# Kernel optimization log

Hardware: AMD Instinct MI355X
Metric: run time of the kernel (lower is better)

## Reference

```python
import jax, jax.numpy as jnp
import numpy as np

D_MODEL = 4096
D_BASE = 8192
K_SUB = 1024
N_TOK = 8192


def setup_inputs() -> dict:
    key = jax.random.key(0)
    k1, k2, k3, k4 = jax.random.split(key, 4)
    x = jax.random.normal(k1, (N_TOK, D_MODEL), dtype=jnp.float32)
    subspace_indices = jax.random.randint(k2, (K_SUB,), 0, D_BASE)
    # learned shared basis (orthogonal init approximated by scaled gaussian)
    U_base = jax.random.normal(k3, (D_MODEL, D_BASE), dtype=jnp.float32) / np.sqrt(D_MODEL)
    V_base = jax.random.normal(k4, (D_BASE, D_MODEL), dtype=jnp.float32) / np.sqrt(D_BASE)
    return {"x": x, "subspace_indices": subspace_indices, "U_base": U_base, "V_base": V_base}


def reference(x, subspace_indices, U_base, V_base):
    # gather active subspace columns/rows of the shared basis
    u_subset = U_base[:, subspace_indices]          # [d_model, k]
    v_subset = V_base[subspace_indices, :]          # [k, d_model]
    projected = jax.nn.silu(x @ u_subset)           # [n_tok, k]
    return projected @ v_subset                     # [n_tok, d_model]
```

## Files before the change

kernel.cpp:

```cpp
#include <hip/hip_runtime.h>
#include <hip/hip_bf16.h>
#include <stdint.h>

#define D_MODEL 4096
#define D_BASE  8192
#define K_SUB   1024
#define N_TOK   8192

typedef __attribute__((ext_vector_type(8))) short bf16x8;
typedef __attribute__((ext_vector_type(4))) float f32x4;

__device__ __forceinline__ unsigned short f2bf(float f) {
    union { float f; uint32_t u; } c; c.f = f;
    uint32_t u = c.u;
    uint32_t r = u + 0x7FFFu + ((u >> 16) & 1u);
    return (unsigned short)(r >> 16);
}

__device__ __forceinline__ void gload_lds16(const void* g, void* l) {
    __builtin_amdgcn_global_load_lds(
        (__attribute__((address_space(1))) void*)g,
        (__attribute__((address_space(3))) void*)l, 16, 0, 0);
}

#define VMCNT(N) do { __builtin_amdgcn_sched_barrier(0); \
    asm volatile("s_waitcnt vmcnt(" #N ")" ::: "memory"); } while (0)
#define PHASE_MID() do { __builtin_amdgcn_sched_barrier(0); __builtin_amdgcn_s_barrier(); \
    asm volatile("s_waitcnt lgkmcnt(0)" ::: "memory"); __builtin_amdgcn_sched_barrier(0); } while (0)
#define PHASE_END() do { __builtin_amdgcn_sched_barrier(0); __builtin_amdgcn_s_barrier(); } while (0)

__global__ __launch_bounds__(256) void prep_fused(const float* __restrict__ x,
                                                  const int* __restrict__ idx,
                                                  const float* __restrict__ U,
                                                  const float* __restrict__ V,
                                                  unsigned short* __restrict__ xb,
                                                  unsigned short* __restrict__ Ut,
                                                  unsigned short* __restrict__ Vt) {
    __shared__ __align__(16) char smem[8704];
    const int b = blockIdx.x;
    const int t = threadIdx.x;
    if (b < 2048) {
        unsigned short* tile = (unsigned short*)smem;
        const int n0 = (b & 3) * 256;
        const int k0 = (b >> 2) * 8;
        const int n = n0 + t;
        const int col = idx[n];
        const float* Ucol = U + (size_t)k0 * D_BASE + col;
        #pragma unroll
        for (int kr = 0; kr < 8; ++kr)
            tile[t * 12 + kr] = f2bf(Ucol[(size_t)kr * D_BASE]);
        __syncthreads();
        ushort4 a = *(const ushort4*)&tile[t * 12];
        ushort4 q = *(const ushort4*)&tile[t * 12 + 4];
        *(ushort4*)(Ut + (size_t)n * D_MODEL + k0) = a;
        *(ushort4*)(Ut + (size_t)n * D_MODEL + k0 + 4) = q;
    } else if (b < 3072) {
        unsigned short (*tile)[66] = (unsigned short(*)[66])smem;
        int* lidx = (int*)(smem + 64 * 66 * 2);
        const int bx = b - 2048;
        const int n0 = (bx & 15) * 64;
        const int d0 = (bx >> 4) * 64;
        if (t < 64) lidx[t] = idx[n0 + t];
        __syncthreads();
        const int c = t & 63, r4 = t >> 6;
        #pragma unroll
        for (int p = 0; p < 16; ++p) {
            int nr = p * 4 + r4;
            tile[nr][c] = f2bf(V[(size_t)lidx[nr] * D_MODEL + d0 + c]);
        }
        __syncthreads();
        #pragma unroll
        for (int p = 0; p < 16; ++p) {
            int dr = p * 4 + r4;
            Vt[(size_t)(d0 + dr) * K_SUB + n0 + c] = tile[c][dr];
        }
    } else {
        const int cb = b - 3072;
        int e = cb * 256 + t;
        const float4* p = (const float4*)x + (size_t)e * 2;
        float4 a = p[0], q = p[1];
        ushort4 lo, hi;
        lo.x = f2bf(a.x); lo.y = f2bf(a.y); lo.z = f2bf(a.z); lo.w = f2bf(a.w);
        hi.x = f2bf(q.x); hi.y = f2bf(q.y); hi.z = f2bf(q.z); hi.w = f2bf(q.w);
        *(ushort4*)(xb + (size_t)e * 8) = lo;
        *(ushort4*)(xb + (size_t)e * 8 + 4) = hi;
    }
}

__global__ __launch_bounds__(512, 2)
void gemm1_8p(const unsigned short* __restrict__ A, const unsigned short* __restrict__ Bt,
              unsigned short* __restrict__ C) {
    constexpr int K = D_MODEL, N = K_SUB, NT = K / 64;
    __shared__ __align__(16) unsigned short lds[49152];

    const int t = threadIdx.x, lane = t & 63, w = t >> 6;
    const int wm = w >> 1, wn = w & 1;
    const int lr = lane & 15, lk = lane >> 4;

    const int f = blockIdx.x;
    const int g = (f & 7) * 32 + (f >> 3);
    const int m0 = (g >> 3) * 256, n0 = (g & 7) * 128;

    const int cswz0 = ((lk ^ (lr & 7)) * 8);
    const int cswz1 = (((4 + lk) ^ (lr & 7)) * 8);
    const int srow = lane >> 3;
    const int scol = ((lane & 7) ^ srow) * 8;

    auto stage_A = [&](int kt, int half) {
        const unsigned short* src = A + (size_t)(m0 + half * 128) * K + kt * 64;
        unsigned short* dst = &lds[(kt & 1) * 24576 + half * 8192];
        #pragma unroll
        for (int i = 0; i < 2; ++i) {
            int c2 = i * 8 + w;
            gload_lds16(src + (size_t)(c2 * 8 + srow) * K + scol, dst + c2 * 512);
        }
    };
    auto stage_B = [&](int kt) {
        const unsigned short* src = Bt + (size_t)n0 * K + kt * 64;
        unsigned short* dst = &lds[(kt & 1) * 24576 + 16384];
        #pragma unroll
        for (int i = 0; i < 2; ++i) {
            int c2 = i * 8 + w;
            gload_lds16(src + (size_t)(c2 * 8 + srow) * K + scol, dst + c2 * 512);
        }
    };
    auto read_A = [&](int kt, bf16x8 (&af)[4][2]) {
        const unsigned short* base = &lds[(kt & 1) * 24576 + (wm >> 1) * 8192];
        #pragma unroll
        for (int m = 0; m < 4; ++m) {
            int rw = (wm & 1) * 64 + m * 16 + lr;
            af[m][0] = *(const bf16x8*)(base + rw * 64 + cswz0);
            af[m][1] = *(const bf16x8*)(base + rw * 64 + cswz1);
        }
    };
    auto read_B2 = [&](int kt, int nh, bf16x8 (&bfr)[2][2]) {
        const unsigned short* base = &lds[(kt & 1) * 24576 + 16384];
        #pragma unroll
        for (int n = 0; n < 2; ++n) {
            int rw = wn * 64 + (nh * 2 + n) * 16 + lr;
            bfr[n][0] = *(const bf16x8*)(base + rw * 64 + cswz0);
            bfr[n][1] = *(const bf16x8*)(base + rw * 64 + cswz1);
        }
    };

    f32x4 acc[4][4] = {};

    stage_A(0, 0); stage_A(0, 1); stage_B(0); stage_A(1, 0);
    VMCNT(2);
    __builtin_amdgcn_s_barrier();
    __builtin_amdgcn_sched_barrier(0);

    for (int kt = 0; kt < NT; kt += 2) {
        const bool more = (kt + 2 < NT);
        {
            bf16x8 af[4][2], bfr[2][2];
            read_A(kt, af); read_B2(kt, 0, bfr);
            stage_A(kt + 1, 1); stage_B(kt + 1);
            PHASE_MID();
            __builtin_amdgcn_s_setprio(1);
            #pragma unroll
            for (int m = 0; m < 4; ++m)
                #pragma unroll
                for (int n = 0; n < 2; ++n)
                    #pragma unroll
                    for (int ks = 0; ks < 2; ++ks)
                        acc[m][n] = __builtin_amdgcn_mfma_f32_16x16x32_bf16(
                            af[m][ks], bfr[n][ks], acc[m][n], 0, 0, 0);
            __builtin_amdgcn_s_setprio(0);
            PHASE_END();
            bf16x8 bfr2[2][2];
            read_B2(kt, 1, bfr2);
            if (more) stage_A(kt + 2, 0);
            PHASE_MID();
            __builtin_amdgcn_s_setprio(1);
            #pragma unroll
            for (int m = 0; m < 4; ++m)
                #pragma unroll
                for (int n = 0; n < 2; ++n)
                    #pragma unroll
                    for (int ks = 0; ks < 2; ++ks)
                        acc[m][2 + n] = __builtin_amdgcn_mfma_f32_16x16x32_bf16(
                            af[m][ks], bfr2[n][ks], acc[m][2 + n], 0, 0, 0);
            __builtin_amdgcn_s_setprio(0);
            if (more) { VMCNT(2); } else { VMCNT(0); }
            PHASE_END();
        }
        {
            bf16x8 af[4][2], bfr[2][2];
            read_A(kt + 1, af); read_B2(kt + 1, 0, bfr);
            if (more) { stage_A(kt + 2, 1); stage_B(kt + 2); }
            PHASE_MID();
            __builtin_amdgcn_s_setprio(1);
            #pragma unroll
            for (int m = 0; m < 4; ++m)
                #pragma unroll
                for (int n = 0; n < 2; ++n)
                    #pragma unroll
                    for (int ks = 0; ks < 2; ++ks)
                        acc[m][n] = __builtin_amdgcn_mfma_f32_16x16x32_bf16(
                            af[m][ks], bfr[n][ks], acc[m][n], 0, 0, 0);
            __builtin_amdgcn_s_setprio(0);
            PHASE_END();
            bf16x8 bfr2[2][2];
            read_B2(kt + 1, 1, bfr2);
            if (more) stage_A(kt + 3, 0);
            PHASE_MID();
            __builtin_amdgcn_s_setprio(1);
            #pragma unroll
            for (int m = 0; m < 4; ++m)
                #pragma unroll
                for (int n = 0; n < 2; ++n)
                    #pragma unroll
                    for (int ks = 0; ks < 2; ++ks)
                        acc[m][2 + n] = __builtin_amdgcn_mfma_f32_16x16x32_bf16(
                            af[m][ks], bfr2[n][ks], acc[m][2 + n], 0, 0, 0);
            __builtin_amdgcn_s_setprio(0);
            if (more) VMCNT(2);
            PHASE_END();
        }
    }

    #pragma unroll
    for (int m = 0; m < 4; ++m)
        #pragma unroll
        for (int n = 0; n < 4; ++n)
            #pragma unroll
            for (int r = 0; r < 4; ++r) {
                int row = m0 + wm * 64 + m * 16 + lk * 4 + r;
                int col = n0 + wn * 64 + n * 16 + lr;
                float v = acc[m][n][r];
                v = v / (1.0f + __expf(-v));
                C[(size_t)row * N + col] = f2bf(v);
            }
}

__global__ __launch_bounds__(512, 2)
void gemm2_8p(const unsigned short* __restrict__ A, const unsigned short* __restrict__ Bt,
              float* __restrict__ C) {
    constexpr int K = K_SUB, N = D_MODEL, NT = K / 64;
    constexpr int BUFSZ = 32768;
    __shared__ __align__(16) unsigned short lds[2 * BUFSZ];

    const int t = threadIdx.x, lane = t & 63, w = t >> 6;
    const int wr = w >> 2, wc = w & 3;
    const int lr = lane & 15, lk = lane >> 4;

    const int f = blockIdx.x;
    const int g = (f & 7) * 64 + (f >> 3);
    const int m0 = (g >> 4) * 256, n0 = (g & 15) * 256;

    const int cswz0 = ((lk ^ (lr & 7)) * 8);
    const int cswz1 = (((4 + lk) ^ (lr & 7)) * 8);
    const int srow = lane >> 3;
    const int scol = ((lane & 7) ^ srow) * 8;

    auto stage_A = [&](int kt, int mh) {
        const unsigned short* src = A + (size_t)(m0 + mh * 128) * K + kt * 64;
        unsigned short* dst = &lds[(kt & 1) * BUFSZ + mh * 8192];
        #pragma unroll
        for (int i = 0; i < 2; ++i) {
            int c2 = i * 8 + w;
            gload_lds16(src + (size_t)(c2 * 8 + srow) * K + scol, dst + c2 * 512);
        }
    };
    auto stage_B = [&](int kt, int nh) {
        const unsigned short* src = Bt + (size_t)(n0 + nh * 128) * K + kt * 64;
        unsigned short* dst = &lds[(kt & 1) * BUFSZ + 16384 + nh * 8192];
        #pragma unroll
        for (int i = 0; i < 2; ++i) {
            int c2 = i * 8 + w;
            gload_lds16(src + (size_t)(c2 * 8 + srow) * K + scol, dst + c2 * 512);
        }
    };
    auto read_A = [&](int kt, int mh, bf16x8 (&af)[4][2]) {
        const unsigned short* base = &lds[(kt & 1) * BUFSZ + mh * 8192];
        #pragma unroll
        for (int m = 0; m < 4; ++m) {
            int rw = wr * 64 + m * 16 + lr;
            af[m][0] = *(const bf16x8*)(base + rw * 64 + cswz0);
            af[m][1] = *(const bf16x8*)(base + rw * 64 + cswz1);
        }
    };
    auto read_B = [&](int kt, int nh, bf16x8 (&bfr)[2][2]) {
        const unsigned short* base = &lds[(kt & 1) * BUFSZ + 16384 + nh * 8192];
        #pragma unroll
        for (int n = 0; n < 2; ++n) {
            int rw = wc * 32 + n * 16 + lr;
            bfr[n][0] = *(const bf16x8*)(base + rw * 64 + cswz0);
            bfr[n][1] = *(const bf16x8*)(base + rw * 64 + cswz1);
        }
    };

    f32x4 acc[8][4] = {};

    stage_A(0, 0); stage_B(0, 0); stage_B(0, 1); stage_A(0, 1);
    stage_A(1, 0); stage_B(1, 1); stage_A(1, 1);
    VMCNT(6);
    __builtin_amdgcn_s_barrier();
    __builtin_amdgcn_sched_barrier(0);

    for (int kt = 0; kt < NT; ++kt) {
        bf16x8 af[4][2], bf0[2][2], bf1[2][2];
        {
            read_A(kt, 0, af); read_B(kt, 0, bf0);
            if (kt + 1 < NT) stage_B(kt + 1, 0);
            PHASE_MID();
            __builtin_amdgcn_s_setprio(1);
            #pragma unroll
            for (int m = 0; m < 4; ++m)
                #pragma unroll
                for (int n = 0; n < 2; ++n)
                    #pragma unroll
                    for (int ks = 0; ks < 2; ++ks)
                        acc[m][n] = __builtin_amdgcn_mfma_f32_16x16x32_bf16(
                            af[m][ks], bf0[n][ks], acc[m][n], 0, 0, 0);
            __builtin_amdgcn_s_setprio(0);
            PHASE_END();
        }
        {
            read_B(kt, 1, bf1);
            if (kt + 2 < NT) stage_A(kt + 2, 0);
            PHASE_MID();
            __builtin_amdgcn_s_setprio(1);
            #pragma unroll
            for (int m = 0; m < 4; ++m)
                #pragma unroll
                for (int n = 0; n < 2; ++n)
                    #pragma unroll
                    for (int ks = 0; ks < 2; ++ks)
                        acc[m][2 + n] = __builtin_amdgcn_mfma_f32_16x16x32_bf16(
                            af[m][ks], bf1[n][ks], acc[m][2 + n], 0, 0, 0);
            __builtin_amdgcn_s_setprio(0);
            PHASE_END();
        }
        {
            read_A(kt, 1, af);
            if (kt + 2 < NT) stage_B(kt + 2, 1);
            PHASE_MID();
            __builtin_amdgcn_s_setprio(1);
            #pragma unroll
            for (int m = 0; m < 4; ++m)
                #pragma unroll
                for (int n = 0; n < 2; ++n)
                    #pragma unroll
                    for (int ks = 0; ks < 2; ++ks)
                        acc[4 + m][n] = __builtin_amdgcn_mfma_f32_16x16x32_bf16(
                            af[m][ks], bf0[n][ks], acc[4 + m][n], 0, 0, 0);
            __builtin_amdgcn_s_setprio(0);
            PHASE_END();
        }
        {
            if (kt + 2 < NT) stage_A(kt + 2, 1);
            PHASE_MID();
            __builtin_amdgcn_s_setprio(1);
            #pragma unroll
            for (int m = 0; m < 4; ++m)
                #pragma unroll
                for (int n = 0; n < 2; ++n)
                    #pragma unroll
                    for (int ks = 0; ks < 2; ++ks)
                        acc[4 + m][2 + n] = __builtin_amdgcn_mfma_f32_16x16x32_bf16(
                            af[m][ks], bf1[n][ks], acc[4 + m][2 + n], 0, 0, 0);
            __builtin_amdgcn_s_setprio(0);
            __builtin_amdgcn_sched_barrier(0);
            if (kt < NT - 2) { VMCNT(6); }
            else if (kt == NT - 2) { VMCNT(0); }
            PHASE_END();
        }
    }

    #pragma unroll
    for (int mh = 0; mh < 2; ++mh)
        #pragma unroll
        for (int nh = 0; nh < 2; ++nh)
            #pragma unroll
            for (int m = 0; m < 4; ++m)
                #pragma unroll
                for (int n = 0; n < 2; ++n)
                    #pragma unroll
                    for (int r = 0; r < 4; ++r) {
                        int row = m0 + mh * 128 + wr * 64 + m * 16 + lk * 4 + r;
                        int col = n0 + nh * 128 + wc * 32 + n * 16 + lr;
                        C[(size_t)row * N + col] = acc[mh * 4 + m][nh * 2 + n][r];
                    }
}

extern "C" void kernel_launch(void* const* d_in, const int* in_sizes, int n_in,
                              void* d_out, int out_size, void* d_ws, size_t ws_size,
                              hipStream_t stream) {
    const float* x   = (const float*)d_in[0];
    const int*   idx = (const int*)d_in[1];
    const float* U   = (const float*)d_in[2];
    const float* V   = (const float*)d_in[3];
    float* out = (float*)d_out;

    unsigned short* Ut = (unsigned short*)d_ws;
    unsigned short* Vt = Ut + (size_t)K_SUB * D_MODEL;
    unsigned short* P  = Vt + (size_t)K_SUB * D_MODEL;
    unsigned short* xb = (unsigned short*)d_out;

    prep_fused<<<2048 + 1024 + 16384, 256, 0, stream>>>(x, idx, U, V, xb, Ut, Vt);
    gemm1_8p<<<256, 512, 0, stream>>>(xb, Ut, P);
    gemm2_8p<<<512, 512, 0, stream>>>(P, Vt, out);
}
```

Baseline: 231.3 us.

## Fuse fp32-to-bf16 conversion of x into first GEMM's A-tile load

Removes the separate conversion pass over x in the prep kernel. The first GEMM now loads fp32 x tiles into registers, converts them to bf16 and writes them swizzled into LDS, with a one-stage register prefetch. This saves writing and re-reading a 64 MB bf16 copy of x. In exchange the GEMM reads twice the bytes for A per tile, cannot use direct global-to-LDS loads for A, and carries more registers, with the occupancy hint in the launch bounds dropped. It also removes the LDS round trip in the U gather.

```diff
diff --git a/kernel.cpp b/kernel.cpp
--- a/kernel.cpp
+++ b/kernel.cpp
@@ -8,6 +8,7 @@
 #define N_TOK   8192
 
 typedef __attribute__((ext_vector_type(8))) short bf16x8;
+typedef __attribute__((ext_vector_type(8))) unsigned short u16x8;
 typedef __attribute__((ext_vector_type(4))) float f32x4;
 
 __device__ __forceinline__ unsigned short f2bf(float f) {
@@ -29,32 +30,30 @@
     asm volatile("s_waitcnt lgkmcnt(0)" ::: "memory"); __builtin_amdgcn_sched_barrier(0); } while (0)
 #define PHASE_END() do { __builtin_amdgcn_sched_barrier(0); __builtin_amdgcn_s_barrier(); } while (0)
 
-__global__ __launch_bounds__(256) void prep_fused(const float* __restrict__ x,
-                                                  const int* __restrict__ idx,
+__global__ __launch_bounds__(256) void prep_fused(const int* __restrict__ idx,
                                                   const float* __restrict__ U,
                                                   const float* __restrict__ V,
-                                                  unsigned short* __restrict__ xb,
                                                   unsigned short* __restrict__ Ut,
                                                   unsigned short* __restrict__ Vt) {
     __shared__ __align__(16) char smem[8704];
     const int b = blockIdx.x;
     const int t = threadIdx.x;
     if (b < 2048) {
-        unsigned short* tile = (unsigned short*)smem;
         const int n0 = (b & 3) * 256;
         const int k0 = (b >> 2) * 8;
         const int n = n0 + t;
         const int col = idx[n];
         const float* Ucol = U + (size_t)k0 * D_BASE + col;
+        unsigned short v[8];
         #pragma unroll
         for (int kr = 0; kr < 8; ++kr)
-            tile[t * 12 + kr] = f2bf(Ucol[(size_t)kr * D_BASE]);
-        __syncthreads();
-        ushort4 a = *(const ushort4*)&tile[t * 12];
-        ushort4 q = *(const ushort4*)&tile[t * 12 + 4];
+            v[kr] = f2bf(Ucol[(size_t)kr * D_BASE]);
+        ushort4 a, q;
+        a.x = v[0]; a.y = v[1]; a.z = v[2]; a.w = v[3];
+        q.x = v[4]; q.y = v[5]; q.z = v[6]; q.w = v[7];
         *(ushort4*)(Ut + (size_t)n * D_MODEL + k0) = a;
         *(ushort4*)(Ut + (size_t)n * D_MODEL + k0 + 4) = q;
-    } else if (b < 3072) {
+    } else {
         unsigned short (*tile)[66] = (unsigned short(*)[66])smem;
         int* lidx = (int*)(smem + 64 * 66 * 2);
         const int bx = b - 2048;
@@ -74,28 +73,19 @@
             int dr = p * 4 + r4;
             Vt[(size_t)(d0 + dr) * K_SUB + n0 + c] = tile[c][dr];
         }
-    } else {
-        const int cb = b - 3072;
-        int e = cb * 256 + t;
-        const float4* p = (const float4*)x + (size_t)e * 2;
-        float4 a = p[0], q = p[1];
-        ushort4 lo, hi;
-        lo.x = f2bf(a.x); lo.y = f2bf(a.y); lo.z = f2bf(a.z); lo.w = f2bf(a.w);
-        hi.x = f2bf(q.x); hi.y = f2bf(q.y); hi.z = f2bf(q.z); hi.w = f2bf(q.w);
-        *(ushort4*)(xb + (size_t)e * 8) = lo;
-        *(ushort4*)(xb + (size_t)e * 8 + 4) = hi;
     }
 }
 
-__global__ __launch_bounds__(512, 2)
-void gemm1_8p(const unsigned short* __restrict__ A, const unsigned short* __restrict__ Bt,
-              unsigned short* __restrict__ C) {
+__global__ __launch_bounds__(512)
+void gemm1_f(const float* __restrict__ A, const unsigned short* __restrict__ Bt,
+             unsigned short* __restrict__ C) {
     constexpr int K = D_MODEL, N = K_SUB, NT = K / 64;
     __shared__ __align__(16) unsigned short lds[49152];
 
     const int t = threadIdx.x, lane = t & 63, w = t >> 6;
     const int wm = w >> 1, wn = w & 1;
     const int lr = lane & 15, lk = lane >> 4;
+    const int rt = t >> 1, ch = t & 1;
 
     const int f = blockIdx.x;
     const int g = (f & 7) * 32 + (f >> 3);
@@ -106,13 +96,23 @@
     const int srow = lane >> 3;
     const int scol = ((lane & 7) ^ srow) * 8;
 
-    auto stage_A = [&](int kt, int half) {
-        const unsigned short* src = A + (size_t)(m0 + half * 128) * K + kt * 64;
-        unsigned short* dst = &lds[(kt & 1) * 24576 + half * 8192];
-        #pragma unroll
-        for (int i = 0; i < 2; ++i) {
-            int c2 = i * 8 + w;
-            gload_lds16(src + (size_t)(c2 * 8 + srow) * K + scol, dst + c2 * 512);
+    auto issue_A = [&](int kt, f32x4 (&ar)[8]) {
+        const float* src = A + (size_t)(m0 + rt) * K + kt * 64 + ch * 32;
+        #pragma unroll
+        for (int j = 0; j < 8; ++j)
+            ar[j] = *(const f32x4*)(src + j * 4);
+    };
+    auto write_A = [&](int kt, const f32x4 (&ar)[8]) {
+        unsigned short* dst = &lds[(kt & 1) * 24576 + (rt >> 7) * 8192 + (rt & 127) * 64];
+        const int rsw = rt & 7;
+        #pragma unroll
+        for (int j = 0; j < 4; ++j) {
+            u16x8 v;
+            v[0] = f2bf(ar[2 * j][0]); v[1] = f2bf(ar[2 * j][1]);
+            v[2] = f2bf(ar[2 * j][2]); v[3] = f2bf(ar[2 * j][3]);
+            v[4] = f2bf(ar[2 * j + 1][0]); v[5] = f2bf(ar[2 * j + 1][1]);
+            v[6] = f2bf(ar[2 * j + 1][2]); v[7] = f2bf(ar[2 * j + 1][3]);
+            *(u16x8*)(dst + (((ch * 4 + j) ^ rsw) * 8)) = v;
         }
     };
     auto stage_B = [&](int kt) {
@@ -144,18 +144,22 @@
     };
 
     f32x4 acc[4][4] = {};
-
-    stage_A(0, 0); stage_A(0, 1); stage_B(0); stage_A(1, 0);
-    VMCNT(2);
+    f32x4 ar[8];
+
+    issue_A(0, ar);
+    stage_B(0);
+    write_A(0, ar);
+    issue_A(1, ar);
+    VMCNT(8);
+    asm volatile("s_waitcnt lgkmcnt(0)" ::: "memory");
     __builtin_amdgcn_s_barrier();
     __builtin_amdgcn_sched_barrier(0);
 
-    for (int kt = 0; kt < NT; kt += 2) {
-        const bool more = (kt + 2 < NT);
-        {
-            bf16x8 af[4][2], bfr[2][2];
+    for (int kt = 0; kt < NT; ++kt) {
+        bf16x8 af[4][2], bfr[2][2];
+        {
             read_A(kt, af); read_B2(kt, 0, bfr);
-            stage_A(kt + 1, 1); stage_B(kt + 1);
+            if (kt + 1 < NT) stage_B(kt + 1);
             PHASE_MID();
             __builtin_amdgcn_s_setprio(1);
             #pragma unroll
@@ -168,9 +172,14 @@
                             af[m][ks], bfr[n][ks], acc[m][n], 0, 0, 0);
             __builtin_amdgcn_s_setprio(0);
             PHASE_END();
+        }
+        {
             bf16x8 bfr2[2][2];
             read_B2(kt, 1, bfr2);
-            if (more) stage_A(kt + 2, 0);
+            if (kt + 1 < NT) write_A(kt + 1, ar);
+            if (kt + 2 < NT) issue_A(kt + 2, ar);
+            if (kt + 2 < NT)      { VMCNT(8); }
+            else if (kt + 1 < NT) { VMCNT(0); }
             PHASE_MID();
             __builtin_amdgcn_s_setprio(1);
             #pragma unroll
@@ -182,40 +191,6 @@
                         acc[m][2 + n] = __builtin_amdgcn_mfma_f32_16x16x32_bf16(
                             af[m][ks], bfr2[n][ks], acc[m][2 + n], 0, 0, 0);
             __builtin_amdgcn_s_setprio(0);
-            if (more) { VMCNT(2); } else { VMCNT(0); }
-            PHASE_END();
-        }
-        {
-            bf16x8 af[4][2], bfr[2][2];
-            read_A(kt + 1, af); read_B2(kt + 1, 0, bfr);
-            if (more) { stage_A(kt + 2, 1); stage_B(kt + 2); }
-            PHASE_MID();
-            __builtin_amdgcn_s_setprio(1);
-            #pragma unroll
-            for (int m = 0; m < 4; ++m)
-                #pragma unroll
-                for (int n = 0; n < 2; ++n)
-                    #pragma unroll
-                    for (int ks = 0; ks < 2; ++ks)
-                        acc[m][n] = __builtin_amdgcn_mfma_f32_16x16x32_bf16(
-                            af[m][ks], bfr[n][ks], acc[m][n], 0, 0, 0);
-            __builtin_amdgcn_s_setprio(0);
-            PHASE_END();
-            bf16x8 bfr2[2][2];
-            read_B2(kt + 1, 1, bfr2);
-            if (more) stage_A(kt + 3, 0);
-            PHASE_MID();
-            __builtin_amdgcn_s_setprio(1);
-            #pragma unroll
-            for (int m = 0; m < 4; ++m)
-                #pragma unroll
-                for (int n = 0; n < 2; ++n)
-                    #pragma unroll
-                    for (int ks = 0; ks < 2; ++ks)
-                        acc[m][2 + n] = __builtin_amdgcn_mfma_f32_16x16x32_bf16(
-                            af[m][ks], bfr2[n][ks], acc[m][2 + n], 0, 0, 0);
-            __builtin_amdgcn_s_setprio(0);
-            if (more) VMCNT(2);
             PHASE_END();
         }
     }
@@ -397,9 +372,8 @@
     unsigned short* Ut = (unsigned short*)d_ws;
     unsigned short* Vt = Ut + (size_t)K_SUB * D_MODEL;
     unsigned short* P  = Vt + (size_t)K_SUB * D_MODEL;
-    unsigned short* xb = (unsigned short*)d_out;
-
-    prep_fused<<<2048 + 1024 + 16384, 256, 0, stream>>>(x, idx, U, V, xb, Ut, Vt);
-    gemm1_8p<<<256, 512, 0, stream>>>(xb, Ut, P);
+
+    prep_fused<<<2048 + 1024, 256, 0, stream>>>(idx, U, V, Ut, Vt);
+    gemm1_f<<<256, 512, 0, stream>>>(x, Ut, P);
     gemm2_8p<<<512, 512, 0, stream>>>(P, Vt, out);
 }
```

Measured after the change: 342.0 us. +47.9%, slower.
